# Kernel tuning notes

Hardware: AMD Instinct MI355X
Metric: run time of the kernel (lower is better)

## Reference

```python
import jax, jax.numpy as jnp
import numpy as np

N_VARS = 2048
D_GRAPH = 256
NUM_ADJ = 7
ALPHA = 0.9
MASK = 0.5


def setup_inputs() -> dict:
    key = jax.random.key(0)
    ks = jax.random.split(key, 8)
    init_adj = jax.random.uniform(ks[0], (N_VARS, N_VARS), dtype=jnp.float32, minval=-1.0, maxval=1.0)
    emb1 = jax.random.normal(ks[1], (NUM_ADJ, N_VARS, D_GRAPH), dtype=jnp.float32)
    emb2 = jax.random.normal(ks[2], (NUM_ADJ, N_VARS, D_GRAPH), dtype=jnp.float32)
    lim = 1.0 / np.sqrt(D_GRAPH)
    w1 = jax.random.uniform(ks[3], (NUM_ADJ, D_GRAPH, D_GRAPH), dtype=jnp.float32, minval=-lim, maxval=lim)
    b1 = jax.random.uniform(ks[4], (NUM_ADJ, D_GRAPH), dtype=jnp.float32, minval=-lim, maxval=lim)
    w2 = jax.random.uniform(ks[5], (NUM_ADJ, D_GRAPH, D_GRAPH), dtype=jnp.float32, minval=-lim, maxval=lim)
    b2 = jax.random.uniform(ks[6], (NUM_ADJ, D_GRAPH), dtype=jnp.float32, minval=-lim, maxval=lim)
    time_indices = jax.random.randint(ks[7], (8,), 0, NUM_ADJ)
    return {
        'init_adj': init_adj, 'emb1': emb1, 'emb2': emb2,
        'w1': w1, 'b1': b1, 'w2': w2, 'b2': b2,
        'time_indices': time_indices, 'current_epoch': 10,
    }


def reference(init_adj, emb1, emb2, w1, b1, w2, b2, time_indices, current_epoch):
    n = init_adj.shape[0]
    k = int(n * n * MASK)
    prop = min(current_epoch / 5, ALPHA)  # static python scalar schedule
    eye = jnp.eye(n, dtype=init_adj.dtype)

    def build_one(e1, e2, W1, B1, W2, B2):
        # nn.Linear: x @ W.T + b, then tanh
        nv1 = jnp.tanh(e1 @ W1.T + B1)          # [n, d]
        nv2 = jnp.tanh(e2 @ W2.T + B2)          # [n, d]
        a = (1.0 - prop) * init_adj + prop * (nv1 @ nv2.T)  # [n, n]
        adj = jax.nn.relu(jnp.tanh(a))
        adj = adj * (1.0 - eye)                 # remove diagonal
        flat = adj.reshape(-1)
        _, idx = jax.lax.top_k(flat, k)         # data-dependent sparsification
        m = jnp.zeros_like(flat).at[idx].set(1.0)
        adj = m.reshape(n, n) * adj
        adj = adj + eye
        return adj / adj.sum(axis=1, keepdims=True)  # row-degree normalize

    oadj = jax.vmap(build_one)(emb1, emb2, w1, b1, w2, b2)  # [num_adj, n, n]
    return oadj[time_indices]  # [B, n, n]
```

## Files before the change

### kernel.cpp

```cpp
#include <hip/hip_runtime.h>
#include <cstdint>
#include <cstddef>

#define NVARS 2048
#define DG    256
#define NSLOT 8
#define NN2   (NVARS*NVARS)
#define K_SEL 2097152u
#define CAP   (1u<<18)
#define KS    512

typedef __attribute__((ext_vector_type(8))) short short8;
typedef __attribute__((ext_vector_type(8))) unsigned short ushort8;
typedef __attribute__((ext_vector_type(4))) float floatx4;

__device__ __align__(16) unsigned short g_ebig[NSLOT][2][NVARS*KS];
__device__ __align__(16) unsigned short g_wbig[NSLOT][2][DG*KS];
__device__ __align__(16) unsigned short g_abig[NSLOT][NVARS*KS];
__device__ __align__(16) unsigned short g_bbig[NSLOT][NVARS*KS];
__device__ unsigned g_hist[NSLOT][2048];
__device__ unsigned g_cand[NSLOT][CAP];
__device__ unsigned g_state[NSLOT][16];
__device__ float g_scal[2];

__device__ __forceinline__ unsigned fkey(float x){
  unsigned b = __float_as_uint(x);
  return (b & 0x80000000u) ? ~b : (b | 0x80000000u);
}
__device__ __forceinline__ unsigned short f2bf(float v){
  unsigned u = __float_as_uint(v);
  return (unsigned short)((u + 0x7FFFu + ((u >> 16) & 1u)) >> 16);
}
__device__ __forceinline__ void async16(void* lds, const void* g){
  __builtin_amdgcn_global_load_lds(
      (const __attribute__((address_space(1))) unsigned int*)g,
      (__attribute__((address_space(3))) unsigned int*)lds, 16, 0, 0);
}

__global__ __launch_bounds__(256) void k_prep(const int* __restrict__ tind,
                                              const int* __restrict__ epoch_p){
  int tid = threadIdx.x;
  if (tid < NSLOT){
    int t = tind[tid];
    int fo = tid;
    for (int b = 0; b < tid; b++){ if (tind[b] == t){ fo = b; break; } }
    g_state[tid][0] = (fo == tid) ? 1u : 0u;
    g_state[tid][1] = (unsigned)fo;
    g_state[tid][2] = 0u;
    g_state[tid][3] = K_SEL;
    g_state[tid][4] = 0u;
    g_state[tid][7] = 0x7FFFFFFFu;
    g_state[tid][8] = 0u;
  }
  if (tid == 0){
    double pd = (double)epoch_p[0] / 5.0;
    if (pd > 0.9) pd = 0.9;
    g_scal[0] = (float)(1.0 - pd);
    g_scal[1] = (float)pd;
  }
  unsigned* h = (unsigned*)g_hist;
  for (int i = tid; i < NSLOT*2048; i += 256) h[i] = 0u;
}

__global__ __launch_bounds__(256) void k_split(
    const float* __restrict__ emb1, const float* __restrict__ emb2,
    const float* __restrict__ w1,  const float* __restrict__ w2,
    const int* __restrict__ tind){
  int z = blockIdx.z; int s = z >> 1; int side = z & 1;
  if (!g_state[s][0]) return;
  int t = tind[s];
  int flat = blockIdx.x*256 + threadIdx.x;
  const float* src;
  unsigned short* dst;
  if (flat < 65536){
    int row = flat >> 5, g8 = flat & 31;
    src = (side ? emb2 : emb1) + (size_t)t*NVARS*DG + (size_t)row*DG + g8*8;
    dst = g_ebig[s][side] + (size_t)row*KS + g8*8;
  } else {
    int f2 = flat - 65536;
    int row = f2 >> 5, g8 = f2 & 31;
    src = (side ? w2 : w1) + (size_t)t*DG*DG + (size_t)row*DG + g8*8;
    dst = g_wbig[s][side] + (size_t)row*KS + g8*8;
  }
  float4 v0 = *(const float4*)src;
  float4 v1 = *(const float4*)(src + 4);
  float a[8] = {v0.x,v0.y,v0.z,v0.w,v1.x,v1.y,v1.z,v1.w};
  ushort8 hi8, lo8;
  #pragma unroll
  for (int j = 0; j < 8; j++){
    unsigned short hb = f2bf(a[j]);
    float hv = __uint_as_float(((unsigned)hb) << 16);
    hi8[j] = hb;
    lo8[j] = f2bf(a[j] - hv);
  }
  *(ushort8*)dst         = hi8;
  *(ushort8*)(dst + 256) = lo8;
}

__global__ __launch_bounds__(256, 2) void k_gemm_nv(
    const float* __restrict__ b1, const float* __restrict__ b2,
    const int* __restrict__ tind){
  int z = blockIdx.z; int s = z >> 1; int side = z & 1;
  if (!g_state[s][0]) return;
  int t = tind[s];
  const unsigned short* __restrict__ A = g_ebig[s][side];
  const unsigned short* __restrict__ B = g_wbig[s][side];
  const float* __restrict__ bias = (side ? b2 : b1) + (size_t)t*DG;
  unsigned short* __restrict__ dst = side ? g_bbig[s] : g_abig[s];
  __shared__ __align__(16) unsigned short As[128*64];
  __shared__ __align__(16) unsigned short Bs[128*64];
  __shared__ __align__(16) float Cs[128][68];
  int tid = threadIdx.x;
  int lane = tid & 63, wv = tid >> 6;
  int rowBase = blockIdx.y*128, colBase = blockIdx.x*128;
  int rW = (wv >> 1)*64, cW = (wv & 1)*64;
  int m = lane & 15, q = lane >> 4;
  int rl = lane >> 3, sl = lane & 7;
  floatx4 acc[4][4] = {};
  for (int p = 0; p < 3; p++){
    int aoff = (p == 1) ? 256 : 0;
    int boff = (p == 2) ? 256 : 0;
    for (int k0 = 0; k0 < 256; k0 += 64){
      #pragma unroll
      for (int t4 = 0; t4 < 4; t4++){
        int rloc = wv*32 + t4*8 + rl;
        int g = sl ^ (rloc & 7);
        async16(&As[(wv*32 + t4*8)*64], A + (size_t)(rowBase + rloc)*KS + aoff + k0 + g*8);
        async16(&Bs[(wv*32 + t4*8)*64], B + (size_t)(colBase + rloc)*KS + boff + k0 + g*8);
      }
      __syncthreads();
      #pragma unroll
      for (int kk = 0; kk < 2; kk++){
        short8 af[4], bfr[4];
        #pragma unroll
        for (int i = 0; i < 4; i++){
          int rA = rW + i*16 + m;
          af[i]  = *(const short8*)&As[rA*64 + (((kk*4 + q) ^ (rA & 7))*8)];
          int rB = cW + i*16 + m;
          bfr[i] = *(const short8*)&Bs[rB*64 + (((kk*4 + q) ^ (rB & 7))*8)];
        }
        #pragma unroll
        for (int i = 0; i < 4; i++)
          #pragma unroll
          for (int j = 0; j < 4; j++)
            acc[i][j] = __builtin_amdgcn_mfma_f32_16x16x32_bf16(af[i], bfr[j], acc[i][j], 0, 0, 0);
      }
      __syncthreads();
    }
  }
  for (int h = 0; h < 2; h++){
    if ((wv & 1) == h){
      #pragma unroll
      for (int i = 0; i < 4; i++)
        #pragma unroll
        for (int j = 0; j < 4; j++)
          #pragma unroll
          for (int r = 0; r < 4; r++)
            Cs[rW + i*16 + q*4 + r][j*16 + m] = acc[i][j][r];
    }
    __syncthreads();
    #pragma unroll
    for (int it = 0; it < 4; it++){
      int row = it*32 + (tid >> 3);
      int c8  = (tid & 7)*8;
      float4 va = *(const float4*)&Cs[row][c8];
      float4 vb = *(const float4*)&Cs[row][c8 + 4];
      float v[8] = {va.x,va.y,va.z,va.w,vb.x,vb.y,vb.z,vb.w};
      int colb = colBase + h*64 + c8;
      ushort8 hi8, lo8;
      #pragma unroll
      for (int j = 0; j < 8; j++){
        float e = tanhf(v[j] + bias[colb + j]);
        unsigned short hb = f2bf(e);
        float hv = __uint_as_float(((unsigned)hb) << 16);
        hi8[j] = hb;
        lo8[j] = f2bf(e - hv);
      }
      unsigned short* rp = dst + (size_t)(rowBase + row)*KS;
      *(ushort8*)(rp + colb)       = hi8;
      *(ushort8*)(rp + 256 + colb) = lo8;
    }
    __syncthreads();
  }
}

__global__ __launch_bounds__(256, 2) void k_gemm_s(const float* __restrict__ init,
                                                   float* __restrict__ out){
  int s = blockIdx.z;
  if (!g_state[s][0]) return;
  const unsigned short* __restrict__ A = g_abig[s];
  const unsigned short* __restrict__ B = g_bbig[s];
  __shared__ __align__(16) unsigned short As[128*64];
  __shared__ __align__(16) unsigned short Bs[128*64];
  __shared__ unsigned hloc[2048];
  int tid = threadIdx.x;
  int lane = tid & 63, wv = tid >> 6;
  int rowBase = blockIdx.y*128, colBase = blockIdx.x*128;
  int rW = (wv >> 1)*64, cW = (wv & 1)*64;
  int m = lane & 15, q = lane >> 4;
  int rl = lane >> 3, sl = lane & 7;
  for (int i = tid; i < 2048; i += 256) hloc[i] = 0u;
  floatx4 acc[4][4] = {};
  for (int p = 0; p < 3; p++){
    int aoff = (p == 1) ? 256 : 0;
    int boff = (p == 2) ? 256 : 0;
    for (int k0 = 0; k0 < 256; k0 += 64){
      #pragma unroll
      for (int t4 = 0; t4 < 4; t4++){
        int rloc = wv*32 + t4*8 + rl;
        int g = sl ^ (rloc & 7);
        async16(&As[(wv*32 + t4*8)*64], A + (size_t)(rowBase + rloc)*KS + aoff + k0 + g*8);
        async16(&Bs[(wv*32 + t4*8)*64], B + (size_t)(colBase + rloc)*KS + boff + k0 + g*8);
      }
      __syncthreads();
      #pragma unroll
      for (int kk = 0; kk < 2; kk++){
        short8 af[4], bfr[4];
        #pragma unroll
        for (int i = 0; i < 4; i++){
          int rA = rW + i*16 + m;
          af[i]  = *(const short8*)&As[rA*64 + (((kk*4 + q) ^ (rA & 7))*8)];
          int rB = cW + i*16 + m;
          bfr[i] = *(const short8*)&Bs[rB*64 + (((kk*4 + q) ^ (rB & 7))*8)];
        }
        #pragma unroll
        for (int i = 0; i < 4; i++)
          #pragma unroll
          for (int j = 0; j < 4; j++)
            acc[i][j] = __builtin_amdgcn_mfma_f32_16x16x32_bf16(af[i], bfr[j], acc[i][j], 0, 0, 0);
      }
      __syncthreads();
    }
  }
  float am1 = g_scal[0], am2 = g_scal[1];
  float* __restrict__ outs = out + (size_t)s*NN2;
  #pragma unroll
  for (int i = 0; i < 4; i++){
    #pragma unroll
    for (int j = 0; j < 4; j++){
      int col = colBase + cW + j*16 + m;
      #pragma unroll
      for (int r = 0; r < 4; r++){
        int row = rowBase + rW + i*16 + q*4 + r;
        float val = am1*init[(size_t)row*NVARS + col] + am2*acc[i][j][r];
        if (row == col) val = -__builtin_inff();
        outs[(size_t)row*NVARS + col] = val;
        atomicAdd(&hloc[fkey(val) >> 21], 1u);
      }
    }
  }
  __syncthreads();
  for (int i = tid; i < 2048; i += 256){
    unsigned c = hloc[i];
    if (c) atomicAdd(&g_hist[s][i], c);
  }
}

__device__ void desc_select(unsigned* h, unsigned* sc, int nb, unsigned rank,
                            unsigned* od, unsigned* orem, unsigned* ocnt){
  int tid = threadIdx.x;
  int per = nb >> 8;
  unsigned loc[8];
  unsigned own = 0;
  int base = tid*per;
  for (int j = 0; j < per; j++){ loc[j] = h[base+j]; own += loc[j]; }
  sc[tid] = own;
  __syncthreads();
  for (int off = 1; off < 256; off <<= 1){
    unsigned v = (tid + off < 256) ? sc[tid+off] : 0u;
    __syncthreads();
    sc[tid] += v;
    __syncthreads();
  }
  unsigned acc = sc[tid] - own;
  for (int j = per-1; j >= 0; j--){
    unsigned c = loc[j];
    if (c && rank > acc && rank <= acc + c){ *od = (unsigned)(base+j); *orem = rank - acc; *ocnt = c; }
    acc += c;
  }
  __syncthreads();
}
__device__ void asc_select(unsigned* h, unsigned* sc, int nb, unsigned rank,
                           unsigned* od, unsigned* orem){
  int tid = threadIdx.x;
  int per = nb >> 8;
  unsigned loc[8];
  unsigned own = 0;
  int base = tid*per;
  for (int j = 0; j < per; j++){ loc[j] = h[base+j]; own += loc[j]; }
  sc[tid] = own;
  __syncthreads();
  for (int off = 1; off < 256; off <<= 1){
    unsigned v = (tid >= off) ? sc[tid-off] : 0u;
    __syncthreads();
    sc[tid] += v;
    __syncthreads();
  }
  unsigned below = sc[tid] - own;
  for (int j = 0; j < per; j++){
    unsigned c = loc[j];
    if (c && rank > below && rank <= below + c){ *od = (unsigned)(base+j); *orem = rank - below; }
    below += c;
  }
  __syncthreads();
}

__global__ __launch_bounds__(256) void k_select1(){
  int s = blockIdx.x;
  if (!g_state[s][0]) return;
  int tid = threadIdx.x;
  __shared__ unsigned h[2048];
  __shared__ unsigned sc[256];
  __shared__ unsigned sd, srem, scnt;
  for (int i = tid; i < 2048; i += 256) h[i] = g_hist[s][i];
  if (tid == 0){ sd = 0; srem = 1; scnt = 1; }
  __syncthreads();
  desc_select(h, sc, 2048, K_SEL, &sd, &srem, &scnt);
  if (tid == 0){ g_state[s][2] = sd << 21; g_state[s][3] = srem; }
}

__global__ __launch_bounds__(256) void k_collect(const float* __restrict__ out){
  int s = blockIdx.z;
  if (!g_state[s][0]) return;
  unsigned pb = g_state[s][2] >> 21;
  const float4* p = (const float4*)(out + (size_t)s*NN2);
  int stride = gridDim.x*256;
  for (int i = blockIdx.x*256 + threadIdx.x; i < NN2/4; i += stride){
    float4 v = p[i];
    float xs[4] = {v.x, v.y, v.z, v.w};
    #pragma unroll
    for (int j = 0; j < 4; j++){
      if ((fkey(xs[j]) >> 21) == pb){
        unsigned pos = atomicAdd(&g_state[s][8], 1u);
        if (pos < CAP) g_cand[s][pos] = (unsigned)(i*4 + j);
      }
    }
  }
}

__global__ __launch_bounds__(256) void k_final(const float* __restrict__ out){
  int s = blockIdx.x;
  if (!g_state[s][0]) return;
  int tid = threadIdx.x;
  unsigned mcnt = g_state[s][8]; if (mcnt > CAP) mcnt = CAP;
  unsigned krem = g_state[s][3];
  unsigned prefix = g_state[s][2];
  const float* outs = out + (size_t)s*NN2;
  __shared__ unsigned h[2048];
  __shared__ unsigned sc[256];
  __shared__ unsigned sd, srem, scnt;
  for (int i = tid; i < 2048; i += 256) h[i] = 0u;
  if (tid == 0){ sd = 0; srem = 1; scnt = 1; }
  __syncthreads();
  for (unsigned i = tid; i < mcnt; i += 256){
    unsigned u = fkey(outs[g_cand[s][i]]);
    atomicAdd(&h[(u >> 10) & 0x7FFu], 1u);
  }
  __syncthreads();
  desc_select(h, sc, 2048, krem, &sd, &srem, &scnt);
  unsigned d1 = sd, krem2 = srem;
  __syncthreads();
  for (int i = tid; i < 2048; i += 256) h[i] = 0u;
  __syncthreads();
  for (unsigned i = tid; i < mcnt; i += 256){
    unsigned u = fkey(outs[g_cand[s][i]]);
    if (((u >> 10) & 0x7FFu) == d1) atomicAdd(&h[u & 0x3FFu], 1u);
  }
  __syncthreads();
  desc_select(h, sc, 1024, krem2, &sd, &srem, &scnt);
  unsigned d0 = sd, nek = srem, cnteq = scnt;
  __syncthreads();
  unsigned tu = prefix | (d1 << 10) | d0;
  unsigned cutoff = 0x7FFFFFFFu;
  if (nek < cnteq){
    for (int i = tid; i < 2048; i += 256) h[i] = 0u;
    __syncthreads();
    for (unsigned i = tid; i < mcnt; i += 256){
      unsigned idx = g_cand[s][i];
      if (fkey(outs[idx]) == tu) atomicAdd(&h[idx >> 11], 1u);
    }
    __syncthreads();
    asc_select(h, sc, 2048, nek, &sd, &srem);
    unsigned dh = sd, j2 = srem;
    __syncthreads();
    for (int i = tid; i < 2048; i += 256) h[i] = 0u;
    __syncthreads();
    for (unsigned i = tid; i < mcnt; i += 256){
      unsigned idx = g_cand[s][i];
      if (fkey(outs[idx]) == tu && (idx >> 11) == dh) atomicAdd(&h[idx & 0x7FFu], 1u);
    }
    __syncthreads();
    asc_select(h, sc, 2048, j2, &sd, &srem);
    cutoff = (dh << 11) | sd;
    __syncthreads();
  }
  if (tid == 0){ g_state[s][4] = tu; g_state[s][7] = cutoff; }
}

__global__ __launch_bounds__(256) void k_masknorm(float* __restrict__ out){
  int s = blockIdx.y;
  if (!g_state[s][0]) return;
  int r = blockIdx.x;
  int tid = threadIdx.x;
  unsigned tu = g_state[s][4];
  unsigned cutoff = g_state[s][7];
  const float4* rowp = (const float4*)(out + (size_t)s*NN2 + (size_t)r*NVARS);
  unsigned baseIdx = (unsigned)(r*NVARS);
  float4 res[2];
  double lsum = 0.0;
  #pragma unroll
  for (int t = 0; t < 2; t++){
    int c4 = tid + t*256;
    float4 a4 = rowp[c4];
    float av[4] = {a4.x, a4.y, a4.z, a4.w};
    float rv[4];
    #pragma unroll
    for (int j = 0; j < 4; j++){
      int c = c4*4 + j;
      float vv;
      if (c == r) vv = 1.0f;
      else {
        unsigned u = fkey(av[j]);
        bool keep = (u > tu) || (u == tu && (baseIdx + (unsigned)c) <= cutoff);
        vv = keep ? fmaxf(tanhf(av[j]), 0.0f) : 0.0f;
      }
      rv[j] = vv;
      lsum += (double)vv;
    }
    res[t].x = rv[0]; res[t].y = rv[1]; res[t].z = rv[2]; res[t].w = rv[3];
  }
  __shared__ double red[256];
  red[tid] = lsum;
  __syncthreads();
  for (int off = 128; off > 0; off >>= 1){
    if (tid < off) red[tid] += red[tid+off];
    __syncthreads();
  }
  float inv = 1.0f / (float)red[0];
  #pragma unroll
  for (int t = 0; t < 2; t++){
    res[t].x *= inv; res[t].y *= inv; res[t].z *= inv; res[t].w *= inv;
  }
  for (int s2 = 0; s2 < NSLOT; s2++){
    if (g_state[s2][1] == (unsigned)s){
      float4* dst = (float4*)(out + (size_t)s2*NN2 + (size_t)r*NVARS);
      dst[tid]       = res[0];
      dst[tid + 256] = res[1];
    }
  }
}

extern "C" void kernel_launch(void* const* d_in, const int* in_sizes, int n_in,
                              void* d_out, int out_size, void* d_ws, size_t ws_size,
                              hipStream_t stream){
  (void)in_sizes; (void)n_in; (void)d_ws; (void)ws_size; (void)out_size;
  const float* init = (const float*)d_in[0];
  const float* emb1 = (const float*)d_in[1];
  const float* emb2 = (const float*)d_in[2];
  const float* w1   = (const float*)d_in[3];
  const float* b1   = (const float*)d_in[4];
  const float* w2   = (const float*)d_in[5];
  const float* b2   = (const float*)d_in[6];
  const int* tind   = (const int*)d_in[7];
  const int* epoch  = (const int*)d_in[8];
  float* out = (float*)d_out;

  k_prep<<<1, 256, 0, stream>>>(tind, epoch);
  k_split<<<dim3(288, 1, 16), 256, 0, stream>>>(emb1, emb2, w1, w2, tind);
  k_gemm_nv<<<dim3(2, 16, 16), 256, 0, stream>>>(b1, b2, tind);
  k_gemm_s<<<dim3(16, 16, 8), 256, 0, stream>>>(init, out);
  k_select1<<<8, 256, 0, stream>>>();
  k_collect<<<dim3(256, 1, 8), 256, 0, stream>>>(out);
  k_final<<<8, 256, 0, stream>>>(out);
  k_masknorm<<<dim3(2048, 8), 256, 0, stream>>>(out);
}
```

Before: 381.8 us.

## Load hi/lo bf16 splits together and stage epilogue through LDS for vector stores

The split-bf16 GEMM now loads the hi and lo halves of both operands into one 128-wide LDS tile per k-step. It issues all three MFMA products (hh, lh, hl) per fragment instead of making three separate passes over K, which cuts global loads and barriers. The epilogue writes accumulators to LDS in two halves, then reads them back row-contiguous so init reads and output writes become float4 vector accesses. LDS use grows to 64KB plus the histogram, which may reduce occupancy below the declared two blocks per CU.

Measured after the change: 346.5 us. 1.1x faster.

```diff
diff --git a/kernel.cpp b/kernel.cpp
--- a/kernel.cpp
+++ b/kernel.cpp
@@ -190,66 +190,95 @@
   if (!g_state[s][0]) return;
   const unsigned short* __restrict__ A = g_abig[s];
   const unsigned short* __restrict__ B = g_bbig[s];
-  __shared__ __align__(16) unsigned short As[128*64];
-  __shared__ __align__(16) unsigned short Bs[128*64];
+  __shared__ __align__(16) unsigned short SM[2][128*128];
   __shared__ unsigned hloc[2048];
+  unsigned short* As = SM[0];
+  unsigned short* Bs = SM[1];
   int tid = threadIdx.x;
   int lane = tid & 63, wv = tid >> 6;
   int rowBase = blockIdx.y*128, colBase = blockIdx.x*128;
   int rW = (wv >> 1)*64, cW = (wv & 1)*64;
   int m = lane & 15, q = lane >> 4;
-  int rl = lane >> 3, sl = lane & 7;
+  int rl4 = lane >> 4;
+  int gl  = lane & 15;
   for (int i = tid; i < 2048; i += 256) hloc[i] = 0u;
   floatx4 acc[4][4] = {};
-  for (int p = 0; p < 3; p++){
-    int aoff = (p == 1) ? 256 : 0;
-    int boff = (p == 2) ? 256 : 0;
-    for (int k0 = 0; k0 < 256; k0 += 64){
-      #pragma unroll
-      for (int t4 = 0; t4 < 4; t4++){
-        int rloc = wv*32 + t4*8 + rl;
-        int g = sl ^ (rloc & 7);
-        async16(&As[(wv*32 + t4*8)*64], A + (size_t)(rowBase + rloc)*KS + aoff + k0 + g*8);
-        async16(&Bs[(wv*32 + t4*8)*64], B + (size_t)(colBase + rloc)*KS + boff + k0 + g*8);
-      }
-      __syncthreads();
-      #pragma unroll
-      for (int kk = 0; kk < 2; kk++){
-        short8 af[4], bfr[4];
+  for (int k0 = 0; k0 < 256; k0 += 64){
+    #pragma unroll
+    for (int t8 = 0; t8 < 8; t8++){
+      int rloc = wv*32 + t8*4 + rl4;
+      int g = (gl & 8) | ((gl ^ rloc) & 7);
+      int off = ((g & 8) ? 256 : 0) + k0 + (g & 7)*8;
+      async16(&As[(wv*32 + t8*4)*128], A + (size_t)(rowBase + rloc)*KS + off);
+      async16(&Bs[(wv*32 + t8*4)*128], B + (size_t)(colBase + rloc)*KS + off);
+    }
+    __syncthreads();
+    #pragma unroll
+    for (int kk = 0; kk < 2; kk++){
+      short8 ah[4], bh[4], al[4], bl[4];
+      #pragma unroll
+      for (int i = 0; i < 4; i++){
+        int rA = rW + i*16 + m;
+        int pa = (kk*4 + q) ^ (rA & 7);
+        ah[i] = *(const short8*)&As[rA*128 + pa*8];
+        al[i] = *(const short8*)&As[rA*128 + (8 + pa)*8];
+        int rB = cW + i*16 + m;
+        int pb = (kk*4 + q) ^ (rB & 7);
+        bh[i] = *(const short8*)&Bs[rB*128 + pb*8];
+        bl[i] = *(const short8*)&Bs[rB*128 + (8 + pb)*8];
+      }
+      #pragma unroll
+      for (int i = 0; i < 4; i++)
         #pragma unroll
-        for (int i = 0; i < 4; i++){
-          int rA = rW + i*16 + m;
-          af[i]  = *(const short8*)&As[rA*64 + (((kk*4 + q) ^ (rA & 7))*8)];
-          int rB = cW + i*16 + m;
-          bfr[i] = *(const short8*)&Bs[rB*64 + (((kk*4 + q) ^ (rB & 7))*8)];
+        for (int j = 0; j < 4; j++){
+          acc[i][j] = __builtin_amdgcn_mfma_f32_16x16x32_bf16(ah[i], bh[j], acc[i][j], 0, 0, 0);
+          acc[i][j] = __builtin_amdgcn_mfma_f32_16x16x32_bf16(al[i], bh[j], acc[i][j], 0, 0, 0);
+          acc[i][j] = __builtin_amdgcn_mfma_f32_16x16x32_bf16(ah[i], bl[j], acc[i][j], 0, 0, 0);
         }
-        #pragma unroll
-        for (int i = 0; i < 4; i++)
-          #pragma unroll
-          for (int j = 0; j < 4; j++)
-            acc[i][j] = __builtin_amdgcn_mfma_f32_16x16x32_bf16(af[i], bfr[j], acc[i][j], 0, 0, 0);
-      }
-      __syncthreads();
-    }
+    }
+    __syncthreads();
   }
   float am1 = g_scal[0], am2 = g_scal[1];
   float* __restrict__ outs = out + (size_t)s*NN2;
-  #pragma unroll
-  for (int i = 0; i < 4; i++){
+  float (*Cs)[68] = (float(*)[68])SM;
+  for (int h = 0; h < 2; h++){
+    if ((wv & 1) == h){
+      #pragma unroll
+      for (int i = 0; i < 4; i++)
+        #pragma unroll
+        for (int j = 0; j < 4; j++)
+          #pragma unroll
+          for (int r = 0; r < 4; r++)
+            Cs[rW + i*16 + q*4 + r][j*16 + m] = acc[i][j][r];
+    }
+    __syncthreads();
     #pragma unroll
-    for (int j = 0; j < 4; j++){
-      int col = colBase + cW + j*16 + m;
-      #pragma unroll
-      for (int r = 0; r < 4; r++){
-        int row = rowBase + rW + i*16 + q*4 + r;
-        float val = am1*init[(size_t)row*NVARS + col] + am2*acc[i][j][r];
-        if (row == col) val = -__builtin_inff();
-        outs[(size_t)row*NVARS + col] = val;
+    for (int it = 0; it < 4; it++){
+      int row = it*32 + (tid >> 3);
+      int c8  = (tid & 7)*8;
+      float4 va = *(const float4*)&Cs[row][c8];
+      float4 vb = *(const float4*)&Cs[row][c8 + 4];
+      float v[8] = {va.x,va.y,va.z,va.w,vb.x,vb.y,vb.z,vb.w};
+      int grow = rowBase + row;
+      int col  = colBase + h*64 + c8;
+      const float* ip = init + (size_t)grow*NVARS + col;
+      float4 i0 = *(const float4*)ip;
+      float4 i1 = *(const float4*)(ip + 4);
+      float iv[8] = {i0.x,i0.y,i0.z,i0.w,i1.x,i1.y,i1.z,i1.w};
+      float o[8];
+      #pragma unroll
+      for (int j = 0; j < 8; j++){
+        float val = am1*iv[j] + am2*v[j];
+        if (grow == col + j) val = -__builtin_inff();
+        o[j] = val;
         atomicAdd(&hloc[fkey(val) >> 21], 1u);
       }
-    }
-  }
-  __syncthreads();
+      float* op = outs + (size_t)grow*NVARS + col;
+      *(float4*)op       = make_float4(o[0], o[1], o[2], o[3]);
+      *(float4*)(op + 4) = make_float4(o[4], o[5], o[6], o[7]);
+    }
+    __syncthreads();
+  }
   for (int i = tid; i < 2048; i += 256){
     unsigned c = hloc[i];
     if (c) atomicAdd(&g_hist[s][i], c);
```
